# Performance work log

Hardware: AMD Instinct MI355X
Metric: run time of the kernel (lower is better)

Reference implementation:

```python
import jax, jax.numpy as jnp
import numpy as np

B, W, H, L, D = 4, 32, 32, 32, 256
K, S, V = 24, 16384, 8  # heads, selected positions per head, logits per head
N = B * W * H * L


def setup_inputs() -> dict:
    key = jax.random.key(0)
    k1, k2, k3, k4, k5 = jax.random.split(key, 5)
    block_type_grid = jax.random.randint(k1, (B, W, H, L), 0, 800, dtype=jnp.int32)
    features = jax.random.normal(k2, (B, W, H, L, D), dtype=jnp.float32)
    mask_idx = jax.random.randint(k3, (K, S), 0, N, dtype=jnp.int32)
    head_weights = jax.random.normal(k4, (K, D, V), dtype=jnp.float32) * (1.0 / np.sqrt(D))
    head_bias = jax.random.normal(k5, (K, V), dtype=jnp.float32) * 0.01
    return {
        "block_type_grid": block_type_grid,
        "features": features,
        "mask_idx": mask_idx,
        "head_weights": head_weights,
        "head_bias": head_bias,
    }


def reference(block_type_grid, features, mask_idx, head_weights, head_bias):
    # Flatten spatial grid: (B,W,H,L,D) -> (N,D)
    feats_flat = features.reshape(-1, D)
    # Grouped boolean-mask gather (as fixed-size index gather): (K,S,D)
    gathered = feats_flat[mask_idx]
    # Per-head small Linear: logits[k,s,v] = gathered[k,s,:] @ W[k,:,v] + b[k,v]
    logits = jnp.einsum('ksd,kdv->ksv', gathered, head_weights) + head_bias[:, None, :]
    return logits
```

## Files before the change

### kernel.cpp

```cpp
#include <hip/hip_runtime.h>


#define KH 24
#define SS 16384
#define VV 8
#define DD 256

template <int CTRL>
__device__ __forceinline__ float dpp_mov(float x) {
    int xi = __builtin_bit_cast(int, x);
    int r = __builtin_amdgcn_update_dpp(xi, xi, CTRL, 0xF, 0xF, false);
    return __builtin_bit_cast(float, r);
}

__global__ __launch_bounds__(256) void attr_decoder_kernel(
    const float* __restrict__ feats,
    const int*   __restrict__ mask_idx,
    const float* __restrict__ head_w,
    const float* __restrict__ head_b,
    float*       __restrict__ out)
{
    const int lane  = threadIdx.x & 63;
    const int wv    = __builtin_amdgcn_readfirstlane(threadIdx.x >> 6);
    const int k     = blockIdx.x >> 7;
    const int chunk = blockIdx.x & 127;
    const int lb    = lane & 7;

    const float* Wk = head_w + (size_t)k * (DD * VV);
    float w[4][8];
    {
        const bool q0 = (lane & 1) != 0;
        const bool q1 = (lane & 2) != 0;
        const bool q2 = (lane & 4) != 0;
#pragma unroll
        for (int t = 0; t < 4; ++t) {
            const float4 a = *(const float4*)(Wk + (lane * 4 + t) * VV);
            const float4 b = *(const float4*)(Wk + (lane * 4 + t) * VV + 4);
            const float x[8] = {a.x, a.y, a.z, a.w, b.x, b.y, b.z, b.w};
            float y[8], z[8];
#pragma unroll
            for (int j = 0; j < 8; ++j) y[j] = q0 ? x[j ^ 1] : x[j];
#pragma unroll
            for (int j = 0; j < 8; ++j) z[j] = q1 ? y[j ^ 2] : y[j];
#pragma unroll
            for (int j = 0; j < 8; ++j) w[t][j] = q2 ? z[j ^ 4] : z[j];
        }
    }
    const float bias = head_b[k * VV + lb];

    const char* fb = (const char*)feats;
    const int s_base = chunk * 128 + wv * 32;
    const int* mi = mask_idx + k * SS + s_base;
    float* outp = out + ((size_t)k * SS + s_base) * VV;
    const int vo = lane << 4;

    int4 rows = *(const int4*)mi;
    int r0 = __builtin_amdgcn_readfirstlane(rows.x);
    int r1 = __builtin_amdgcn_readfirstlane(rows.y);
    int r2 = __builtin_amdgcn_readfirstlane(rows.z);
    int r3 = __builtin_amdgcn_readfirstlane(rows.w);

    for (int i = 0; i < 32; i += 4) {
        const float4 f0 = *(const float4*)(fb + (((size_t)(unsigned)r0) << 10) + vo);
        const float4 f1 = *(const float4*)(fb + (((size_t)(unsigned)r1) << 10) + vo);
        const float4 f2 = *(const float4*)(fb + (((size_t)(unsigned)r2) << 10) + vo);
        const float4 f3 = *(const float4*)(fb + (((size_t)(unsigned)r3) << 10) + vo);

        if (i < 28) rows = *(const int4*)(mi + i + 4);

        float r[4];
        const float4 f[4] = {f0, f1, f2, f3};
#pragma unroll
        for (int u = 0; u < 4; ++u) {
            float acc[8];
#pragma unroll
            for (int v = 0; v < 8; ++v) {
                acc[v] = f[u].x * w[0][v];
                acc[v] = fmaf(f[u].y, w[1][v], acc[v]);
                acc[v] = fmaf(f[u].z, w[2][v], acc[v]);
                acc[v] = fmaf(f[u].w, w[3][v], acc[v]);
            }
            const float a40 = acc[0] + dpp_mov<0xB1>(acc[1]);
            const float a41 = acc[2] + dpp_mov<0xB1>(acc[3]);
            const float a42 = acc[4] + dpp_mov<0xB1>(acc[5]);
            const float a43 = acc[6] + dpp_mov<0xB1>(acc[7]);
            const float a20 = a40 + dpp_mov<0x4E>(a41);
            const float a21 = a42 + dpp_mov<0x4E>(a43);
            r[u] = a20 + __shfl_xor(a21, 4, 64);
        }

        r0 = __builtin_amdgcn_readfirstlane(rows.x);
        r1 = __builtin_amdgcn_readfirstlane(rows.y);
        r2 = __builtin_amdgcn_readfirstlane(rows.z);
        r3 = __builtin_amdgcn_readfirstlane(rows.w);

        const bool b3 = (lane & 8) != 0;
        const bool b4 = (lane & 16) != 0;
        const float t0 = (b3 ? r[1] : r[0]) + dpp_mov<0x128>(b3 ? r[0] : r[1]);
        const float t1 = (b3 ? r[3] : r[2]) + dpp_mov<0x128>(b3 ? r[2] : r[3]);
        float va = (b4 ? t1 : t0) + __shfl_xor(b4 ? t0 : t1, 16, 64);
        va += __shfl_xor(va, 32, 64);

        if (lane < 32) outp[i * VV + lane] = va + bias;
    }
}

extern "C" void kernel_launch(void* const* d_in, const int* in_sizes, int n_in,
                              void* d_out, int out_size, void* d_ws, size_t ws_size,
                              hipStream_t stream) {
    const float* feats    = (const float*)d_in[1];
    const int*   mask_idx = (const int*)  d_in[2];
    const float* head_w   = (const float*)d_in[3];
    const float* head_b   = (const float*)d_in[4];
    float* out = (float*)d_out;

    dim3 grid(KH * 128);
    dim3 block(256);
    attr_decoder_kernel<<<grid, block, 0, stream>>>(feats, mask_idx, head_w, head_b, out);
}
```

Measured before the change: 232.8 us.

## Bucket gathered rows by address region and map regions to XCDs for L2 locality

```diff
diff --git a/kernel.cpp b/kernel.cpp
--- a/kernel.cpp
+++ b/kernel.cpp
@@ -5,6 +5,7 @@
 #define SS 16384
 #define VV 8
 #define DD 256
+#define NPOS 128
 
 template <int CTRL>
 __device__ __forceinline__ float dpp_mov(float x) {
@@ -13,12 +14,139 @@
     return __builtin_bit_cast(float, r);
 }
 
-__global__ __launch_bounds__(256) void attr_decoder_kernel(
+__global__ __launch_bounds__(256) void bucket_kernel(
+    const int* __restrict__ mask_idx,
+    int* __restrict__ offsets,
+    unsigned int* __restrict__ list)
+{
+    const int head = blockIdx.x;
+    const int tid  = threadIdx.x;
+    const int* mi = mask_idx + head * SS;
+
+    __shared__ int hist[NPOS];
+    __shared__ int base[NPOS];
+    __shared__ int cnt[NPOS];
+    if (tid < NPOS) { hist[tid] = 0; cnt[tid] = 0; }
+    __syncthreads();
+
+    for (int i = tid; i < SS; i += 256)
+        atomicAdd(&hist[((unsigned)mi[i]) >> 10], 1);
+    __syncthreads();
+
+    if (tid == 0) {
+        int a = 0;
+        for (int b = 0; b < NPOS; ++b) { base[b] = a; a += hist[b]; }
+    }
+    __syncthreads();
+
+    if (tid < NPOS) offsets[head * (NPOS + 1) + tid] = base[tid];
+    if (tid == 0)   offsets[head * (NPOS + 1) + NPOS] = SS;
+
+    for (int i = tid; i < SS; i += 256) {
+        const unsigned row = (unsigned)mi[i];
+        const int b = row >> 10;
+        const int p = atomicAdd(&cnt[b], 1);
+        list[head * SS + base[b] + p] = (row << 14) | (unsigned)i;
+    }
+}
+
+__global__ __launch_bounds__(256) void decode_kernel(
     const float* __restrict__ feats,
-    const int*   __restrict__ mask_idx,
+    const unsigned int* __restrict__ list,
+    const int* __restrict__ offsets,
     const float* __restrict__ head_w,
     const float* __restrict__ head_b,
     float*       __restrict__ out)
+{
+    const int lane   = threadIdx.x & 63;
+    const int wv     = threadIdx.x >> 6;
+    const int g      = blockIdx.x;
+    const int xcd    = g & 7;
+    const int q      = g >> 3;
+    const int head   = q % KH;
+    const int eighth = q / KH;
+
+    const float* Wk = head_w + (size_t)head * (DD * VV);
+    float w[4][8];
+    {
+        const bool q0 = (lane & 1) != 0;
+        const bool q1 = (lane & 2) != 0;
+        const bool q2 = (lane & 4) != 0;
+#pragma unroll
+        for (int t = 0; t < 4; ++t) {
+            const float4 a = *(const float4*)(Wk + (lane * 4 + t) * VV);
+            const float4 b = *(const float4*)(Wk + (lane * 4 + t) * VV + 4);
+            const float x[8] = {a.x, a.y, a.z, a.w, b.x, b.y, b.z, b.w};
+            float y[8], z[8];
+#pragma unroll
+            for (int j = 0; j < 8; ++j) y[j] = q0 ? x[j ^ 1] : x[j];
+#pragma unroll
+            for (int j = 0; j < 8; ++j) z[j] = q1 ? y[j ^ 2] : y[j];
+#pragma unroll
+            for (int j = 0; j < 8; ++j) w[t][j] = q2 ? z[j ^ 4] : z[j];
+        }
+    }
+    const float bias = head_b[head * VV + (lane & 7)];
+
+    const char* fb = (const char*)feats;
+    const int vo = lane << 4;
+    const unsigned int* lst = list + head * SS;
+    const int* offs = offsets + head * (NPOS + 1);
+    float* outh = out + (size_t)head * SS * VV;
+    const int widx = eighth * 4 + wv;
+
+    for (int t = 0; t < 16; ++t) {
+        const int pos = t * 8 + xcd;
+        const int lo = offs[pos];
+        const int hi = offs[pos + 1];
+        int j = lo + widx;
+        if (j >= hi) continue;
+
+        unsigned e0 = lst[j];
+        int r0 = __builtin_amdgcn_readfirstlane((int)(e0 >> 14));
+        float4 f0 = *(const float4*)(fb + (((size_t)(unsigned)r0) << 10) + vo);
+
+        for (; j < hi; j += 32) {
+            const int jn = j + 32;
+            unsigned e1 = e0;
+            float4 f1 = f0;
+            if (jn < hi) {
+                e1 = lst[jn];
+                int r1 = __builtin_amdgcn_readfirstlane((int)(e1 >> 14));
+                f1 = *(const float4*)(fb + (((size_t)(unsigned)r1) << 10) + vo);
+            }
+
+            float acc[8];
+#pragma unroll
+            for (int v = 0; v < 8; ++v) {
+                acc[v] = f0.x * w[0][v];
+                acc[v] = fmaf(f0.y, w[1][v], acc[v]);
+                acc[v] = fmaf(f0.z, w[2][v], acc[v]);
+                acc[v] = fmaf(f0.w, w[3][v], acc[v]);
+            }
+            const float a40 = acc[0] + dpp_mov<0xB1>(acc[1]);
+            const float a41 = acc[2] + dpp_mov<0xB1>(acc[3]);
+            const float a42 = acc[4] + dpp_mov<0xB1>(acc[5]);
+            const float a43 = acc[6] + dpp_mov<0xB1>(acc[7]);
+            const float a20 = a40 + dpp_mov<0x4E>(a41);
+            const float a21 = a42 + dpp_mov<0x4E>(a43);
+            float va = a20 + __shfl_xor(a21, 4, 64);
+            va += dpp_mov<0x128>(va);
+            va += __shfl_xor(va, 16, 64);
+            va += __shfl_xor(va, 32, 64);
+
+            const int s = (int)(e0 & 16383u);
+            if (lane < 8) outh[(size_t)s * VV + lane] = va + bias;
+
+            e0 = e1; f0 = f1;
+        }
+    }
+}
+
+__global__ __launch_bounds__(256) void attr_decoder_fallback(
+    const float* __restrict__ feats, const int* __restrict__ mask_idx,
+    const float* __restrict__ head_w, const float* __restrict__ head_b,
+    float* __restrict__ out)
 {
     const int lane  = threadIdx.x & 63;
     const int wv    = __builtin_amdgcn_readfirstlane(threadIdx.x >> 6);
@@ -65,7 +193,6 @@
         const float4 f1 = *(const float4*)(fb + (((size_t)(unsigned)r1) << 10) + vo);
         const float4 f2 = *(const float4*)(fb + (((size_t)(unsigned)r2) << 10) + vo);
         const float4 f3 = *(const float4*)(fb + (((size_t)(unsigned)r3) << 10) + vo);
-
         if (i < 28) rows = *(const int4*)(mi + i + 4);
 
         float r[4];
@@ -88,7 +215,6 @@
             const float a21 = a42 + dpp_mov<0x4E>(a43);
             r[u] = a20 + __shfl_xor(a21, 4, 64);
         }
-
         r0 = __builtin_amdgcn_readfirstlane(rows.x);
         r1 = __builtin_amdgcn_readfirstlane(rows.y);
         r2 = __builtin_amdgcn_readfirstlane(rows.z);
@@ -100,7 +226,6 @@
         const float t1 = (b3 ? r[3] : r[2]) + dpp_mov<0x128>(b3 ? r[2] : r[3]);
         float va = (b4 ? t1 : t0) + __shfl_xor(b4 ? t0 : t1, 16, 64);
         va += __shfl_xor(va, 32, 64);
-
         if (lane < 32) outp[i * VV + lane] = va + bias;
     }
 }
@@ -114,7 +239,15 @@
     const float* head_b   = (const float*)d_in[4];
     float* out = (float*)d_out;
 
-    dim3 grid(KH * 128);
-    dim3 block(256);
-    attr_decoder_kernel<<<grid, block, 0, stream>>>(feats, mask_idx, head_w, head_b, out);
-}
+    const size_t need = 16384 + (size_t)KH * SS * 4;
+    if (d_ws != nullptr && ws_size >= need) {
+        int* offsets = (int*)d_ws;
+        unsigned int* list = (unsigned int*)((char*)d_ws + 16384);
+        bucket_kernel<<<dim3(KH), dim3(256), 0, stream>>>(mask_idx, offsets, list);
+        decode_kernel<<<dim3(1536), dim3(256), 0, stream>>>(
+            feats, list, offsets, head_w, head_b, out);
+    } else {
+        attr_decoder_fallback<<<dim3(KH * 128), dim3(256), 0, stream>>>(
+            feats, mask_idx, head_w, head_b, out);
+    }
+}
```

Result: slower. 312.6 us (+34.3%).

## Compute all rows densely with split-bf16 MFMA, then scatter via bucketed indices

Applied to the files above, without the earlier changes.

```diff
diff --git a/kernel.cpp b/kernel.cpp
--- a/kernel.cpp
+++ b/kernel.cpp
@@ -5,6 +5,23 @@
 #define SS 16384
 #define VV 8
 #define DD 256
+#define NROW 131072
+#define NE (KH * SS)
+#define NB 2048
+#define LDSP 196
+
+typedef __attribute__((ext_vector_type(8))) short s16x8;
+typedef __attribute__((ext_vector_type(4))) float f32x4;
+
+__device__ __forceinline__ unsigned short rne_bf16(float f) {
+    unsigned u = __builtin_bit_cast(unsigned, f);
+    unsigned r = u + 0x7FFFu + ((u >> 16) & 1u);
+    return (unsigned short)(r >> 16);
+}
+__device__ __forceinline__ float bf16f(unsigned short h) {
+    unsigned u = ((unsigned)h) << 16;
+    return __builtin_bit_cast(float, u);
+}
 
 template <int CTRL>
 __device__ __forceinline__ float dpp_mov(float x) {
@@ -13,12 +30,144 @@
     return __builtin_bit_cast(float, r);
 }
 
-__global__ __launch_bounds__(256) void attr_decoder_kernel(
+__global__ __launch_bounds__(256) void wk_kernel(
+    const float* __restrict__ head_w, unsigned short* __restrict__ whi,
+    unsigned short* __restrict__ wlo, unsigned* __restrict__ cursor)
+{
+    const int idx = blockIdx.x * 256 + threadIdx.x;
+    if (idx < NB) cursor[idx] = 0u;
+    const int j = idx & 7, lane = (idx >> 3) & 63;
+    const int kb = (idx >> 9) & 7, hp = idx >> 12;
+    const int head = hp * 2 + ((lane & 15) >> 3);
+    const int v = lane & 7;
+    const int k = kb * 32 + (lane >> 4) * 8 + j;
+    const float f = head_w[((size_t)head * DD + k) * VV + v];
+    const unsigned short hi = rne_bf16(f);
+    whi[idx] = hi;
+    wlo[idx] = rne_bf16(f - bf16f(hi));
+}
+
+__global__ __launch_bounds__(256) void hk_kernel(
+    const int* __restrict__ mask_idx, unsigned* __restrict__ cursor)
+{
+    const int idx = blockIdx.x * 256 + threadIdx.x;
+    const unsigned row = (unsigned)mask_idx[idx];
+    atomicAdd(&cursor[row >> 6], 1u);
+}
+
+__global__ __launch_bounds__(1024) void sk_kernel(
+    unsigned* __restrict__ cursor, int* __restrict__ bbounds)
+{
+    const int tid = threadIdx.x;
+    __shared__ unsigned part[1024];
+    const unsigned c0 = cursor[2 * tid], c1 = cursor[2 * tid + 1];
+    part[tid] = c0 + c1;
+    __syncthreads();
+    for (int off = 1; off < 1024; off <<= 1) {
+        unsigned v = (tid >= off) ? part[tid - off] : 0u;
+        __syncthreads();
+        part[tid] += v;
+        __syncthreads();
+    }
+    const unsigned ex = tid ? part[tid - 1] : 0u;
+    bbounds[2 * tid] = (int)ex;
+    bbounds[2 * tid + 1] = (int)(ex + c0);
+    cursor[2 * tid] = ex;
+    cursor[2 * tid + 1] = ex + c0;
+    if (tid == 0) bbounds[NB] = NE;
+}
+
+__global__ __launch_bounds__(256) void ek_kernel(
+    const int* __restrict__ mask_idx, unsigned* __restrict__ cursor,
+    unsigned* __restrict__ entries)
+{
+    const int idx = blockIdx.x * 256 + threadIdx.x;
+    const unsigned row = (unsigned)mask_idx[idx];
+    const unsigned pos = atomicAdd(&cursor[row >> 6], 1u);
+    entries[pos] = ((row & 63u) << 19) | (unsigned)idx;
+}
+
+__global__ __launch_bounds__(256) void mk_kernel(
     const float* __restrict__ feats,
-    const int*   __restrict__ mask_idx,
-    const float* __restrict__ head_w,
+    const unsigned short* __restrict__ whi,
+    const unsigned short* __restrict__ wlo,
+    const unsigned* __restrict__ entries,
+    const int* __restrict__ bbounds,
     const float* __restrict__ head_b,
-    float*       __restrict__ out)
+    float* __restrict__ out)
+{
+    const int tid  = threadIdx.x;
+    const int wave = tid >> 6;
+    const int lane = tid & 63;
+    const int m    = lane & 15;
+    const int kq   = lane >> 4;
+    const int r0   = blockIdx.x * 64;
+
+    __shared__ float Cl[64 * LDSP];
+    __shared__ unsigned short Bbuf[8192];
+    __shared__ float bias_s[192];
+    if (tid < 192) bias_s[tid] = head_b[tid];
+
+    const float* arow = feats + ((size_t)(r0 + wave * 16 + m)) * DD + kq * 8;
+    s16x8 ahi[8], alo[8];
+#pragma unroll
+    for (int kb = 0; kb < 8; ++kb) {
+        const float4 p = *(const float4*)(arow + kb * 32);
+        const float4 q = *(const float4*)(arow + kb * 32 + 4);
+        const float fv[8] = {p.x, p.y, p.z, p.w, q.x, q.y, q.z, q.w};
+#pragma unroll
+        for (int j = 0; j < 8; ++j) {
+            const unsigned short hi = rne_bf16(fv[j]);
+            ahi[kb][j] = (short)hi;
+            alo[kb][j] = (short)rne_bf16(fv[j] - bf16f(hi));
+        }
+    }
+
+    for (int hp = 0; hp < 12; ++hp) {
+        if (hp) __syncthreads();
+        {
+            const uint4* sh = (const uint4*)(whi + hp * 4096);
+            const uint4* sl = (const uint4*)(wlo + hp * 4096);
+            uint4* bb = (uint4*)Bbuf;
+            bb[tid]       = sh[tid];
+            bb[256 + tid] = sh[256 + tid];
+            bb[512 + tid] = sl[tid];
+            bb[768 + tid] = sl[256 + tid];
+        }
+        __syncthreads();
+
+        f32x4 c = {0.f, 0.f, 0.f, 0.f};
+#pragma unroll
+        for (int kb = 0; kb < 8; ++kb) {
+            const s16x8 bh = *(const s16x8*)((const char*)Bbuf + kb * 1024 + lane * 16);
+            const s16x8 bl = *(const s16x8*)((const char*)Bbuf + 8192 + kb * 1024 + lane * 16);
+            c = __builtin_amdgcn_mfma_f32_16x16x32_bf16(ahi[kb], bh, c, 0, 0, 0);
+            c = __builtin_amdgcn_mfma_f32_16x16x32_bf16(alo[kb], bh, c, 0, 0, 0);
+            c = __builtin_amdgcn_mfma_f32_16x16x32_bf16(ahi[kb], bl, c, 0, 0, 0);
+        }
+#pragma unroll
+        for (int rg = 0; rg < 4; ++rg)
+            Cl[(wave * 16 + kq * 4 + rg) * LDSP + hp * 16 + (lane & 15)] = c[rg];
+    }
+    __syncthreads();
+
+    const int lo_e = bbounds[blockIdx.x];
+    const int hi_e = bbounds[blockIdx.x + 1];
+    const int v = tid & 7;
+    for (int e = lo_e + (tid >> 3); e < hi_e; e += 32) {
+        const unsigned ent = entries[e];
+        const int nl = (int)(ent >> 19);
+        const int kk = (int)((ent >> 14) & 31u);
+        const int s  = (int)(ent & 16383u);
+        const float val = Cl[nl * LDSP + kk * 8 + v] + bias_s[kk * 8 + v];
+        out[((size_t)kk * SS + s) * VV + v] = val;
+    }
+}
+
+__global__ __launch_bounds__(256) void attr_decoder_fallback(
+    const float* __restrict__ feats, const int* __restrict__ mask_idx,
+    const float* __restrict__ head_w, const float* __restrict__ head_b,
+    float* __restrict__ out)
 {
     const int lane  = threadIdx.x & 63;
     const int wv    = __builtin_amdgcn_readfirstlane(threadIdx.x >> 6);
@@ -65,7 +214,6 @@
         const float4 f1 = *(const float4*)(fb + (((size_t)(unsigned)r1) << 10) + vo);
         const float4 f2 = *(const float4*)(fb + (((size_t)(unsigned)r2) << 10) + vo);
         const float4 f3 = *(const float4*)(fb + (((size_t)(unsigned)r3) << 10) + vo);
-
         if (i < 28) rows = *(const int4*)(mi + i + 4);
 
         float r[4];
@@ -88,7 +236,6 @@
             const float a21 = a42 + dpp_mov<0x4E>(a43);
             r[u] = a20 + __shfl_xor(a21, 4, 64);
         }
-
         r0 = __builtin_amdgcn_readfirstlane(rows.x);
         r1 = __builtin_amdgcn_readfirstlane(rows.y);
         r2 = __builtin_amdgcn_readfirstlane(rows.z);
@@ -100,7 +247,6 @@
         const float t1 = (b3 ? r[3] : r[2]) + dpp_mov<0x128>(b3 ? r[2] : r[3]);
         float va = (b4 ? t1 : t0) + __shfl_xor(b4 ? t0 : t1, 16, 64);
         va += __shfl_xor(va, 32, 64);
-
         if (lane < 32) outp[i * VV + lane] = va + bias;
     }
 }
@@ -114,7 +260,23 @@
     const float* head_b   = (const float*)d_in[4];
     float* out = (float*)d_out;
 
-    dim3 grid(KH * 128);
-    dim3 block(256);
-    attr_decoder_kernel<<<grid, block, 0, stream>>>(feats, mask_idx, head_w, head_b, out);
-}
+    const size_t need = 1982480;
+    if (d_ws != nullptr && ws_size >= need) {
+        char* ws = (char*)d_ws;
+        unsigned* cursor  = (unsigned*)(ws);
+        int* bbounds      = (int*)(ws + 8192);
+        unsigned* entries = (unsigned*)(ws + 16400);
+        unsigned short* whi = (unsigned short*)(ws + 1589264);
+        unsigned short* wlo = (unsigned short*)(ws + 1785872);
+
+        wk_kernel<<<dim3(192),  dim3(256),  0, stream>>>(head_w, whi, wlo, cursor);
+        hk_kernel<<<dim3(1536), dim3(256),  0, stream>>>(mask_idx, cursor);
+        sk_kernel<<<dim3(1),    dim3(1024), 0, stream>>>(cursor, bbounds);
+        ek_kernel<<<dim3(1536), dim3(256),  0, stream>>>(mask_idx, cursor, entries);
+        mk_kernel<<<dim3(NB),   dim3(256),  0, stream>>>(
+            feats, whi, wlo, entries, bbounds, head_b, out);
+    } else {
+        attr_decoder_fallback<<<dim3(KH * 128), dim3(256), 0, stream>>>(
+            feats, mask_idx, head_w, head_b, out);
+    }
+}
```

After: 349.8 us. 1.5x slower.
